# Optimization experiments

Measured on AMD Instinct MI355X. Metric: run time of the kernel, lower is better.

Reference implementation:

```python
import jax, jax.numpy as jnp
import numpy as np

B, T, N_EMBD, HEAD = 4, 4096, 1024, 64


def setup_inputs() -> dict:
    key = jax.random.key(0)
    kx, kk, kq, kv = jax.random.split(key, 4)
    x = jax.random.normal(kx, (B, T, N_EMBD), dtype=jnp.float32)
    s = 1.0 / np.sqrt(N_EMBD)  # init scale so activations stay O(1)
    Wk = jax.random.normal(kk, (N_EMBD, HEAD), dtype=jnp.float32) * s
    Wq = jax.random.normal(kq, (N_EMBD, HEAD), dtype=jnp.float32) * s
    Wv = jax.random.normal(kv, (N_EMBD, HEAD), dtype=jnp.float32) * s
    return {"x": x, "Wk": Wk, "Wq": Wq, "Wv": Wv}


def reference(x, Wk, Wq, Wv):
    Bd, Td, C = x.shape
    k = jnp.einsum('btc,ch->bth', x, Wk)
    q = jnp.einsum('btc,ch->bth', x, Wq)
    v = jnp.einsum('btc,ch->bth', x, Wv)
    # scores scaled by C**-0.5 where C = n_embd (as in the source, not head_size)
    w = jnp.einsum('bth,bsh->bts', q, k) * (C ** -0.5)
    causal = jnp.tril(jnp.ones((Td, Td), dtype=bool))  # [T, T]
    w = jnp.where(causal, w, -jnp.inf)
    w = jax.nn.softmax(w, axis=-1)
    out = jnp.einsum('bts,bsh->bth', w, v)  # [B, T, head_size]
    return out
```

## Files before the change

### kernel.cpp

```cpp
#include <hip/hip_runtime.h>
#include <cmath>

#define NB 4
#define NT 4096
#define NC 1024
#define NH 64
#define SCALE 0.03125f
#define MFIX 3.0f
#define LOG2E 1.4426950408889634f
#define NSPLIT 8

typedef __attribute__((ext_vector_type(8))) short v8s;
typedef __attribute__((ext_vector_type(4))) float f32x4;

static __device__ __forceinline__ ushort f2bf(float x) {
    union { float f; uint u; } c; c.f = x;
    return (ushort)((c.u + 0x7FFF + ((c.u >> 16) & 1)) >> 16);
}
static __device__ __forceinline__ float bf2f(ushort h) {
    union { uint u; float f; } c; c.u = (uint)h << 16;
    return c.f;
}

__global__ __launch_bounds__(256) void prep_kernel(
    const float* __restrict__ Wk, const float* __restrict__ Wq,
    const float* __restrict__ Wv, ushort* __restrict__ Wb)
{
    const int g    = blockIdx.x * 256 + threadIdx.x;
    const int lane = g & 63;
    const int kc   = (g >> 6) & 31;
    const int nt   = g >> 11;
    const int n    = nt * 16 + (lane & 15);
    const float* W = (n < 64) ? Wq : (n < 128) ? Wk : Wv;
    const int col  = n & 63;
    const int k0   = kc * 32 + ((lane >> 4) << 3);
    ushort t8[8];
    #pragma unroll
    for (int j = 0; j < 8; ++j)
        t8[j] = f2bf(W[(k0 + j) * 64 + col]);
    *(uint4*)(Wb + (size_t)g * 8) = *(const uint4*)t8;
}

#define PPAD 72

__global__ __launch_bounds__(256) void proj_kernel(
    const float* __restrict__ x, const ushort* __restrict__ Wb,
    ushort* __restrict__ q, ushort* __restrict__ k, ushort* __restrict__ v)
{
    __shared__ ushort As[2][32 * PPAD];
    __shared__ ushort Cs[32][200];

    const int tid  = threadIdx.x;
    const int w    = tid >> 6;
    const int lane = tid & 63;
    const int ln   = lane & 15;
    const int quad = lane >> 4;
    const long r0  = (long)blockIdx.x * 32;

    const int arow = tid >> 3, acol = (tid & 7) * 8;
    const float* xs = x + (r0 + arow) * NC + acol;

    const ushort* wb0 = Wb + (size_t)(w * 3 + 0) * 16384 + lane * 8;
    const ushort* wb1 = Wb + (size_t)(w * 3 + 1) * 16384 + lane * 8;
    const ushort* wb2 = Wb + (size_t)(w * 3 + 2) * 16384 + lane * 8;

    f32x4 acc[2][3];
    #pragma unroll
    for (int s = 0; s < 2; ++s)
        #pragma unroll
        for (int nt = 0; nt < 3; ++nt) acc[s][nt] = (f32x4){0.f,0.f,0.f,0.f};

    float4 f0 = *(const float4*)(xs);
    float4 f1 = *(const float4*)(xs + 4);
    v8s b[3][2];
    b[0][0] = *(const v8s*)(wb0);       b[0][1] = *(const v8s*)(wb0 + 512);
    b[1][0] = *(const v8s*)(wb1);       b[1][1] = *(const v8s*)(wb1 + 512);
    b[2][0] = *(const v8s*)(wb2);       b[2][1] = *(const v8s*)(wb2 + 512);
    {
        ushort t8[8] = { f2bf(f0.x), f2bf(f0.y), f2bf(f0.z), f2bf(f0.w),
                         f2bf(f1.x), f2bf(f1.y), f2bf(f1.z), f2bf(f1.w) };
        *(uint4*)(&As[0][arow * PPAD + acol]) = *(const uint4*)t8;
    }
    __syncthreads();

    int buf = 0;
    #pragma unroll
    for (int it = 0; it < 16; ++it) {
        float4 g0, g1;
        v8s nb[3][2];
        if (it < 15) {
            const int k1 = (it + 1) * 64;
            g0 = *(const float4*)(xs + k1);
            g1 = *(const float4*)(xs + k1 + 4);
            const int off = (it + 1) * 1024;
            nb[0][0] = *(const v8s*)(wb0 + off); nb[0][1] = *(const v8s*)(wb0 + off + 512);
            nb[1][0] = *(const v8s*)(wb1 + off); nb[1][1] = *(const v8s*)(wb1 + off + 512);
            nb[2][0] = *(const v8s*)(wb2 + off); nb[2][1] = *(const v8s*)(wb2 + off + 512);
        }

        #pragma unroll
        for (int s = 0; s < 2; ++s) {
            const ushort* ap = &As[buf][(s * 16 + ln) * PPAD + quad * 8];
            v8s a0 = *(const v8s*)(ap);
            v8s a1 = *(const v8s*)(ap + 32);
            #pragma unroll
            for (int nt = 0; nt < 3; ++nt) {
                acc[s][nt] = __builtin_amdgcn_mfma_f32_16x16x32_bf16(a0, b[nt][0], acc[s][nt], 0, 0, 0);
                acc[s][nt] = __builtin_amdgcn_mfma_f32_16x16x32_bf16(a1, b[nt][1], acc[s][nt], 0, 0, 0);
            }
        }

        if (it < 15) {
            ushort t8[8] = { f2bf(g0.x), f2bf(g0.y), f2bf(g0.z), f2bf(g0.w),
                             f2bf(g1.x), f2bf(g1.y), f2bf(g1.z), f2bf(g1.w) };
            *(uint4*)(&As[buf ^ 1][arow * PPAD + acol]) = *(const uint4*)t8;
            #pragma unroll
            for (int nt = 0; nt < 3; ++nt) {
                b[nt][0] = nb[nt][0];
                b[nt][1] = nb[nt][1];
            }
        }
        __syncthreads();
        buf ^= 1;
    }

    #pragma unroll
    for (int s = 0; s < 2; ++s)
        #pragma unroll
        for (int nt = 0; nt < 3; ++nt)
            #pragma unroll
            for (int r = 0; r < 4; ++r)
                Cs[s * 16 + quad * 4 + r][(w * 3 + nt) * 16 + ln] = f2bf(acc[s][nt][r]);
    __syncthreads();

    const int orow = tid >> 3, oseg = (tid & 7) * 8;
    uint4 u0 = *(const uint4*)(&Cs[orow][oseg]);
    uint4 u1 = *(const uint4*)(&Cs[orow][64 + oseg]);
    uint4 u2 = *(const uint4*)(&Cs[orow][128 + oseg]);
    *(uint4*)(q + (r0 + orow) * NH + oseg) = u0;
    *(uint4*)(k + (r0 + orow) * NH + oseg) = u1;
    *(uint4*)(v + (r0 + orow) * NH + oseg) = u2;
}

#define LPAD 72

__global__ __launch_bounds__(256) void attn_kernel(
    const ushort* __restrict__ q, const ushort* __restrict__ k,
    const ushort* __restrict__ v, ushort* __restrict__ Op, float* __restrict__ Lp)
{
    __shared__ ushort Ks[64 * LPAD];
    __shared__ ushort Vt[64 * LPAD];
    __shared__ ushort Ps[4 * 32 * LPAD];

    const int id = blockIdx.x;
    const int qt = 31 - (id >> 5);
    const int c  = (id >> 2) & 7;
    const int b  = id & 3;
    const int q0 = qt * 128;

    const int tid  = threadIdx.x;
    const int w    = tid >> 6;
    const int lane = tid & 63;
    const int ln   = lane & 15;
    const int quad = lane >> 4;
    const int qw0  = q0 + w * 32;

    const ushort* qb = q + (size_t)b * NT * NH;
    const ushort* kb = k + (size_t)b * NT * NH;
    const ushort* vb = v + (size_t)b * NT * NH;

    v8s qf[2][2];
    #pragma unroll
    for (int s = 0; s < 2; ++s) {
        const ushort* qp = qb + (size_t)(qw0 + s * 16 + ln) * NH + quad * 8;
        qf[s][0] = *(const v8s*)(qp);
        qf[s][1] = *(const v8s*)(qp + 32);
    }

    f32x4 o[2][4];
    #pragma unroll
    for (int s = 0; s < 2; ++s)
        #pragma unroll
        for (int td = 0; td < 4; ++td) o[s][td] = (f32x4){0.f,0.f,0.f,0.f};
    float l[2][4] = {};

    const int nkt   = 2 * qt + 2;
    const int cs    = (nkt + NSPLIT - 1) / NSPLIT;
    const int kt_lo = c * cs;
    const int kt_hi = min(nkt, kt_lo + cs);

    ushort* Pw = Ps + w * 32 * LPAD;

    uint4 kreg0, kreg1, vreg0, vreg1;
    const int kp = tid & 31, dh = tid >> 5;
    const int krow0 = tid >> 3, kc0 = (tid & 7) * 8;
    const int krow1 = (tid + 256) >> 3, kc1 = ((tid + 256) & 7) * 8;

    auto load_tile = [&](int kt) {
        const uint4* kg = (const uint4*)(kb + (size_t)kt * 64 * NH);
        kreg0 = kg[tid];
        kreg1 = kg[tid + 256];
        const ushort* v0 = vb + ((size_t)kt * 64 + 2 * kp) * NH + dh * 8;
        vreg0 = *(const uint4*)(v0);
        vreg1 = *(const uint4*)(v0 + NH);
    };

    if (kt_lo < kt_hi) load_tile(kt_lo);

    for (int kt = kt_lo; kt < kt_hi; ++kt) {
        __syncthreads();
        *(uint4*)(&Ks[krow0 * LPAD + kc0]) = kreg0;
        *(uint4*)(&Ks[krow1 * LPAD + kc1]) = kreg1;
        {
            ushort ra[8], rb[8];
            *(uint4*)(ra) = vreg0;
            *(uint4*)(rb) = vreg1;
            #pragma unroll
            for (int d = 0; d < 8; ++d)
                *(uint*)(&Vt[(dh * 8 + d) * LPAD + 2 * kp]) =
                    (uint)ra[d] | ((uint)rb[d] << 16);
        }
        if (kt + 1 < kt_hi) load_tile(kt + 1);
        __syncthreads();

        #pragma unroll
        for (int tk = 0; tk < 4; ++tk) {
            v8s kf0 = *(const v8s*)(&Ks[(tk * 16 + ln) * LPAD + quad * 8]);
            v8s kf1 = *(const v8s*)(&Ks[(tk * 16 + ln) * LPAD + 32 + quad * 8]);
            const int sg = kt * 64 + tk * 16 + ln;
            #pragma unroll
            for (int s = 0; s < 2; ++s) {
                f32x4 acc = (f32x4){0.f,0.f,0.f,0.f};
                acc = __builtin_amdgcn_mfma_f32_16x16x32_bf16(qf[s][0], kf0, acc, 0, 0, 0);
                acc = __builtin_amdgcn_mfma_f32_16x16x32_bf16(qf[s][1], kf1, acc, 0, 0, 0);
                const bool needmask = (kt * 64 + 63) > (qw0 + s * 16);
                #pragma unroll
                for (int r = 0; r < 4; ++r) {
                    float e = fmaf(acc[r], SCALE * LOG2E, -MFIX * LOG2E);
                    if (needmask) {
                        int qg = qw0 + s * 16 + quad * 4 + r;
                        if (sg > qg) e = -1e30f;
                    }
                    float p = __builtin_amdgcn_exp2f(e);
                    l[s][r] += p;
                    Pw[(s * 16 + quad * 4 + r) * LPAD + tk * 16 + ln] = f2bf(p);
                }
            }
        }

        #pragma unroll
        for (int kc = 0; kc < 2; ++kc) {
            v8s vf[4];
            #pragma unroll
            for (int td = 0; td < 4; ++td)
                vf[td] = *(const v8s*)(&Vt[(td * 16 + ln) * LPAD + kc * 32 + quad * 8]);
            #pragma unroll
            for (int s = 0; s < 2; ++s) {
                v8s pf = *(const v8s*)(&Pw[(s * 16 + ln) * LPAD + kc * 32 + quad * 8]);
                #pragma unroll
                for (int td = 0; td < 4; ++td)
                    o[s][td] = __builtin_amdgcn_mfma_f32_16x16x32_bf16(pf, vf[td], o[s][td], 0, 0, 0);
            }
        }
    }

    float lsum[2][4];
    #pragma unroll
    for (int s = 0; s < 2; ++s)
        #pragma unroll
        for (int r = 0; r < 4; ++r) {
            float x_ = l[s][r];
            x_ += __shfl_xor(x_, 1);
            x_ += __shfl_xor(x_, 2);
            x_ += __shfl_xor(x_, 4);
            x_ += __shfl_xor(x_, 8);
            lsum[s][r] = x_;
        }

    ushort* opc = Op + (size_t)c * NB * NT * NH + (size_t)b * NT * NH;
    float*  lpc = Lp + (size_t)c * NB * NT + (size_t)b * NT;
    #pragma unroll
    for (int s = 0; s < 2; ++s)
        #pragma unroll
        for (int r = 0; r < 4; ++r) {
            const int t = qw0 + s * 16 + quad * 4 + r;
            #pragma unroll
            for (int td = 0; td < 4; ++td)
                opc[(size_t)t * NH + td * 16 + ln] = f2bf(o[s][td][r]);
            if (ln == r) lpc[t] = lsum[s][r];
        }
}

__global__ __launch_bounds__(256) void combine_kernel(
    const ushort* __restrict__ Op, const float* __restrict__ Lp,
    float* __restrict__ out)
{
    const size_t g4 = (size_t)blockIdx.x * 256 + threadIdx.x;
    const size_t h0 = (g4 & 15) * 4;
    const size_t bq = g4 >> 4;
    const size_t QN = (size_t)NB * NT;
    const size_t ON = QN * NH;
    float L = 0.f;
    float o0 = 0.f, o1 = 0.f, o2 = 0.f, o3 = 0.f;
    #pragma unroll
    for (int c = 0; c < NSPLIT; ++c) {
        L += Lp[(size_t)c * QN + bq];
        ushort4 u = *(const ushort4*)(Op + (size_t)c * ON + bq * NH + h0);
        o0 += bf2f(u.x); o1 += bf2f(u.y); o2 += bf2f(u.z); o3 += bf2f(u.w);
    }
    const float inv = 1.f / L;
    float4 r = { o0 * inv, o1 * inv, o2 * inv, o3 * inv };
    *(float4*)(out + bq * NH + h0) = r;
}

extern "C" void kernel_launch(void* const* d_in, const int* in_sizes, int n_in,
                              void* d_out, int out_size, void* d_ws, size_t ws_size,
                              hipStream_t stream)
{
    const float* x  = (const float*)d_in[0];
    const float* Wk = (const float*)d_in[1];
    const float* Wq = (const float*)d_in[2];
    const float* Wv = (const float*)d_in[3];
    float* out = (float*)d_out;

    char* wsb = (char*)d_ws;
    const size_t QE = (size_t)NB * NT * NH;
    ushort* qw = (ushort*)wsb;
    ushort* kw = qw + QE;
    ushort* vw = kw + QE;
    ushort* Wb = vw + QE;
    ushort* Op = (ushort*)(wsb + (8u << 20));
    float*  Lp = (float*)(wsb + (24u << 20));

    prep_kernel<<<96, 256, 0, stream>>>(Wk, Wq, Wv, Wb);
    proj_kernel<<<NB * NT / 32, 256, 0, stream>>>(x, Wb, qw, kw, vw);
    attn_kernel<<<32 * NSPLIT * NB, 256, 0, stream>>>(qw, kw, vw, Op, Lp);
    combine_kernel<<<(int)(QE / 4 / 256), 256, 0, stream>>>(Op, Lp, out);
}
```

Before: 141.5 us.

## Pre-pack K and V into MFMA fragment layout, read directly from global

```diff
diff --git a/kernel.cpp b/kernel.cpp
--- a/kernel.cpp
+++ b/kernel.cpp
@@ -8,7 +8,7 @@
 #define SCALE 0.03125f
 #define MFIX 3.0f
 #define LOG2E 1.4426950408889634f
-#define NSPLIT 8
+#define NSPLIT 12
 
 typedef __attribute__((ext_vector_type(8))) short v8s;
 typedef __attribute__((ext_vector_type(4))) float f32x4;
@@ -45,10 +45,10 @@
 
 __global__ __launch_bounds__(256) void proj_kernel(
     const float* __restrict__ x, const ushort* __restrict__ Wb,
-    ushort* __restrict__ q, ushort* __restrict__ k, ushort* __restrict__ v)
-{
-    __shared__ ushort As[2][32 * PPAD];
-    __shared__ ushort Cs[32][200];
+    ushort* __restrict__ q, ushort* __restrict__ kpack, ushort* __restrict__ vpack)
+{
+    __shared__ __align__(16) ushort As[2][32 * PPAD];
+    __shared__ __align__(16) ushort Cs[32][200];
 
     const int tid  = threadIdx.x;
     const int w    = tid >> 6;
@@ -133,28 +133,48 @@
                 Cs[s * 16 + quad * 4 + r][(w * 3 + nt) * 16 + ln] = f2bf(acc[s][nt][r]);
     __syncthreads();
 
-    const int orow = tid >> 3, oseg = (tid & 7) * 8;
-    uint4 u0 = *(const uint4*)(&Cs[orow][oseg]);
-    uint4 u1 = *(const uint4*)(&Cs[orow][64 + oseg]);
-    uint4 u2 = *(const uint4*)(&Cs[orow][128 + oseg]);
-    *(uint4*)(q + (r0 + orow) * NH + oseg) = u0;
-    *(uint4*)(k + (r0 + orow) * NH + oseg) = u1;
-    *(uint4*)(v + (r0 + orow) * NH + oseg) = u2;
+    const int b_blk = (int)(r0 >> 12);
+    const int t_loc = (int)(r0 & 4095);
+    const int kt    = t_loc >> 6;
+    const int tk0   = (t_loc >> 4) & 3;
+    const int kcb   = (t_loc >> 5) & 1;
+
+    {
+        const int orow = tid >> 3, oseg = (tid & 7) * 8;
+        uint4 u0 = *(const uint4*)(&Cs[orow][oseg]);
+        *(uint4*)(q + (r0 + orow) * NH + oseg) = u0;
+    }
+    {
+        const int tk_loc = tid >> 7, kc = (tid >> 6) & 1, lp = tid & 63;
+        const int lnp = lp & 15, qdp = lp >> 4;
+        uint4 kk = *(const uint4*)(&Cs[tk_loc * 16 + lnp][64 + kc * 32 + qdp * 8]);
+        size_t fid = ((size_t)(b_blk * 64 + kt) * 4 + tk0 + tk_loc) * 2 + kc;
+        *(uint4*)(kpack + fid * 512 + lp * 8) = kk;
+    }
+    {
+        const int td = tid >> 6, lp = tid & 63;
+        const int lnp = lp & 15, qdp = lp >> 4;
+        ushort t8[8];
+        #pragma unroll
+        for (int j = 0; j < 8; ++j)
+            t8[j] = Cs[qdp * 8 + j][128 + td * 16 + lnp];
+        size_t fid = ((size_t)(b_blk * 64 + kt) * 2 + kcb) * 4 + td;
+        *(uint4*)(vpack + fid * 512 + lp * 8) = *(const uint4*)t8;
+    }
 }
 
 #define LPAD 72
 
 __global__ __launch_bounds__(256) void attn_kernel(
-    const ushort* __restrict__ q, const ushort* __restrict__ k,
-    const ushort* __restrict__ v, ushort* __restrict__ Op, float* __restrict__ Lp)
-{
-    __shared__ ushort Ks[64 * LPAD];
-    __shared__ ushort Vt[64 * LPAD];
-    __shared__ ushort Ps[4 * 32 * LPAD];
+    const ushort* __restrict__ q, const ushort* __restrict__ kpack,
+    const ushort* __restrict__ vpack, ushort* __restrict__ Op,
+    float* __restrict__ Lp)
+{
+    __shared__ __align__(16) ushort Ps[4][32 * LPAD];
 
     const int id = blockIdx.x;
-    const int qt = 31 - (id >> 5);
-    const int c  = (id >> 2) & 7;
+    const int qt = 31 - (id / 48);
+    const int c  = (id % 48) >> 2;
     const int b  = id & 3;
     const int q0 = qt * 128;
 
@@ -165,9 +185,9 @@
     const int quad = lane >> 4;
     const int qw0  = q0 + w * 32;
 
-    const ushort* qb = q + (size_t)b * NT * NH;
-    const ushort* kb = k + (size_t)b * NT * NH;
-    const ushort* vb = v + (size_t)b * NT * NH;
+    const ushort* qb  = q + (size_t)b * NT * NH;
+    const ushort* kpb = kpack + (size_t)b * 64 * 8 * 512 + lane * 8;
+    const ushort* vpb = vpack + (size_t)b * 64 * 8 * 512 + lane * 8;
 
     v8s qf[2][2];
     #pragma unroll
@@ -189,44 +209,16 @@
     const int kt_lo = c * cs;
     const int kt_hi = min(nkt, kt_lo + cs);
 
-    ushort* Pw = Ps + w * 32 * LPAD;
-
-    uint4 kreg0, kreg1, vreg0, vreg1;
-    const int kp = tid & 31, dh = tid >> 5;
-    const int krow0 = tid >> 3, kc0 = (tid & 7) * 8;
-    const int krow1 = (tid + 256) >> 3, kc1 = ((tid + 256) & 7) * 8;
-
-    auto load_tile = [&](int kt) {
-        const uint4* kg = (const uint4*)(kb + (size_t)kt * 64 * NH);
-        kreg0 = kg[tid];
-        kreg1 = kg[tid + 256];
-        const ushort* v0 = vb + ((size_t)kt * 64 + 2 * kp) * NH + dh * 8;
-        vreg0 = *(const uint4*)(v0);
-        vreg1 = *(const uint4*)(v0 + NH);
-    };
-
-    if (kt_lo < kt_hi) load_tile(kt_lo);
+    ushort* Pw = &Ps[w][0];
 
     for (int kt = kt_lo; kt < kt_hi; ++kt) {
-        __syncthreads();
-        *(uint4*)(&Ks[krow0 * LPAD + kc0]) = kreg0;
-        *(uint4*)(&Ks[krow1 * LPAD + kc1]) = kreg1;
-        {
-            ushort ra[8], rb[8];
-            *(uint4*)(ra) = vreg0;
-            *(uint4*)(rb) = vreg1;
-            #pragma unroll
-            for (int d = 0; d < 8; ++d)
-                *(uint*)(&Vt[(dh * 8 + d) * LPAD + 2 * kp]) =
-                    (uint)ra[d] | ((uint)rb[d] << 16);
-        }
-        if (kt + 1 < kt_hi) load_tile(kt + 1);
-        __syncthreads();
+        const ushort* kfb = kpb + (size_t)kt * 8 * 512;
+        const ushort* vfb = vpb + (size_t)kt * 8 * 512;
 
         #pragma unroll
         for (int tk = 0; tk < 4; ++tk) {
-            v8s kf0 = *(const v8s*)(&Ks[(tk * 16 + ln) * LPAD + quad * 8]);
-            v8s kf1 = *(const v8s*)(&Ks[(tk * 16 + ln) * LPAD + 32 + quad * 8]);
+            v8s kf0 = *(const v8s*)(kfb + (tk * 2 + 0) * 512);
+            v8s kf1 = *(const v8s*)(kfb + (tk * 2 + 1) * 512);
             const int sg = kt * 64 + tk * 16 + ln;
             #pragma unroll
             for (int s = 0; s < 2; ++s) {
@@ -253,7 +245,7 @@
             v8s vf[4];
             #pragma unroll
             for (int td = 0; td < 4; ++td)
-                vf[td] = *(const v8s*)(&Vt[(td * 16 + ln) * LPAD + kc * 32 + quad * 8]);
+                vf[td] = *(const v8s*)(vfb + (kc * 4 + td) * 512);
             #pragma unroll
             for (int s = 0; s < 2; ++s) {
                 v8s pf = *(const v8s*)(&Pw[(s * 16 + ln) * LPAD + kc * 32 + quad * 8]);
@@ -325,15 +317,15 @@
 
     char* wsb = (char*)d_ws;
     const size_t QE = (size_t)NB * NT * NH;
-    ushort* qw = (ushort*)wsb;
-    ushort* kw = qw + QE;
-    ushort* vw = kw + QE;
-    ushort* Wb = vw + QE;
-    ushort* Op = (ushort*)(wsb + (8u << 20));
-    float*  Lp = (float*)(wsb + (24u << 20));
+    ushort* qw    = (ushort*)wsb;
+    ushort* kpack = qw + QE;
+    ushort* vpack = kpack + QE;
+    ushort* Wb    = vpack + QE;
+    ushort* Op    = (ushort*)(wsb + (8u << 20));
+    float*  Lp    = (float*)(wsb + (40u << 20));
 
     prep_kernel<<<96, 256, 0, stream>>>(Wk, Wq, Wv, Wb);
-    proj_kernel<<<NB * NT / 32, 256, 0, stream>>>(x, Wb, qw, kw, vw);
-    attn_kernel<<<32 * NSPLIT * NB, 256, 0, stream>>>(qw, kw, vw, Op, Lp);
+    proj_kernel<<<NB * NT / 32, 256, 0, stream>>>(x, Wb, qw, kpack, vpack);
+    attn_kernel<<<32 * NSPLIT * NB, 256, 0, stream>>>(qw, kpack, vpack, Op, Lp);
     combine_kernel<<<(int)(QE / 4 / 256), 256, 0, stream>>>(Op, Lp, out);
 }
```

Result: no change. 140.3 us (-0.9%).
